# Kernel optimization log

Hardware: AMD Instinct MI355X
Metric: run time of the kernel (lower is better)

Reference implementation:

```python
import jax, jax.numpy as jnp
import numpy as np

B, S, D, N = 8, 4096, 1024, 64
EPS = 1e-5


def setup_inputs() -> dict:
    key = jax.random.key(0)
    ks = jax.random.split(key, 6)
    sD = 1.0 / np.sqrt(D)
    sN = 1.0 / np.sqrt(N)
    return {
        "x": jax.random.normal(ks[0], (B, S, D), dtype=jnp.float32),
        "ln_w": jnp.ones((D,), jnp.float32),
        "ln_b": jnp.zeros((D,), jnp.float32),
        "Wi": jax.random.normal(ks[1], (N, D), jnp.float32) * sD,
        "bi": jnp.zeros((N,), jnp.float32),
        "Wf": jax.random.normal(ks[2], (N, D), jnp.float32) * sD,
        "bf": jnp.zeros((N,), jnp.float32),
        "Wz": jax.random.normal(ks[3], (N, D), jnp.float32) * sD,
        "bz": jnp.zeros((N,), jnp.float32),
        "Wo": jax.random.normal(ks[4], (N, D), jnp.float32) * sD,
        "bo": jnp.zeros((N,), jnp.float32),
        "Wp": jax.random.normal(ks[5], (D, N), jnp.float32) * sN,
        "bp": jnp.zeros((D,), jnp.float32),
    }


def reference(x, ln_w, ln_b, Wi, bi, Wf, bf, Wz, bz, Wo, bo, Wp, bp):
    # LayerNorm over last dim (eps matches torch default 1e-5)
    mu = jnp.mean(x, axis=-1, keepdims=True)
    var = jnp.mean(jnp.square(x - mu), axis=-1, keepdims=True)
    xn = (x - mu) * jax.lax.rsqrt(var + EPS) * ln_w + ln_b

    # Precompute all four projections as batched GEMMs: (B,S,N)
    log_i = jnp.clip(jnp.einsum('bsd,nd->bsn', xn, Wi) + bi, -20.0, 20.0)
    log_f = jnp.clip(jnp.einsum('bsd,nd->bsn', xn, Wf) + bf, -20.0, 20.0)
    z = jnp.tanh(jnp.einsum('bsd,nd->bsn', xn, Wz) + bz)
    o = jax.nn.sigmoid(jnp.einsum('bsd,nd->bsn', xn, Wo) + bo)

    # Stabilized exponential-gated recurrence via lax.scan over time
    def step(carry, inp):
        c, m = carry
        li, lf, zt, ot = inp
        m_new = jnp.maximum(m + lf, li)
        i_s = jnp.exp(li - m_new)
        f_s = jnp.exp(m + lf - m_new)
        c = f_s * c + i_s * zt
        h = ot * jnp.tanh(c)
        return (c, m_new), h

    c0 = jnp.zeros((x.shape[0], log_i.shape[-1]), x.dtype)
    m0 = jnp.zeros_like(c0)
    # time-major inputs: (S,B,N)
    tm = lambda a: jnp.swapaxes(a, 0, 1)
    _, h_seq = jax.lax.scan(step, (c0, m0), (tm(log_i), tm(log_f), tm(z), tm(o)))
    h_seq = jnp.swapaxes(h_seq, 0, 1)  # (B,S,N)

    return jnp.einsum('bsn,dn->bsd', h_seq, Wp) + bp
```

## Files before the change

kernel.cpp:

```cpp
#include <hip/hip_runtime.h>
#include <hip/hip_bf16.h>

#define BB 8
#define SS 4096
#define DD 1024
#define NN 64
#define ROWS (BB * SS)
#define GLD 256
#define NCHUNK 256
#define CLEN 16

typedef _Float16 f16;
using f16x8 = __attribute__((ext_vector_type(8))) _Float16;
using f32x4 = __attribute__((ext_vector_type(4))) float;

__global__ __launch_bounds__(256) void prep_all(const float* __restrict__ Wi, const float* __restrict__ bi,
                                                const float* __restrict__ Wf, const float* __restrict__ bfv,
                                                const float* __restrict__ Wz, const float* __restrict__ bz,
                                                const float* __restrict__ Wo, const float* __restrict__ bo,
                                                const float* __restrict__ Wp,
                                                const float* __restrict__ ln_w, const float* __restrict__ ln_b,
                                                f16* __restrict__ Wpk, f16* __restrict__ Wpf,
                                                float* __restrict__ ball, float* __restrict__ e_all) {
    if (blockIdx.x < 384) {
        int i = blockIdx.x * 256 + threadIdx.x;
        if (i < 32768) {
            int l = i & 63, cb = (i >> 6) & 15, s = i >> 10;
            int r = cb * 16 + (l & 15);
            int c = s * 32 + (l >> 4) * 8;
            int g = r >> 6, rem = r & 63;
            const float* W = (g == 0) ? Wi : (g == 1) ? Wf : (g == 2) ? Wz : Wo;
            const float* src = W + rem * 1024 + c;
            const float* lwp = ln_w + c;
            f16x8 v;
            #pragma unroll
            for (int e = 0; e < 8; ++e) v[e] = (f16)(src[e] * lwp[e]);
            *reinterpret_cast<f16x8*>(Wpk + (size_t)s * 8192 + cb * 512 + l * 8) = v;
        } else if (i < 32768 + 65536) {
            int j = i - 32768;
            Wpf[j] = (f16)Wp[j];
        }
    } else {
        int j = (blockIdx.x - 384) * 4 + (threadIdx.x >> 6);
        int lane = threadIdx.x & 63;
        int g = j >> 6, rem = j & 63;
        const float* W  = (g == 0) ? Wi : (g == 1) ? Wf : (g == 2) ? Wz : Wo;
        const float* bs = (g == 0) ? bi : (g == 1) ? bfv : (g == 2) ? bz : bo;
        const float* row = W + rem * 1024;
        float d = 0.0f, e = 0.0f;
        #pragma unroll
        for (int t = 0; t < 16; ++t) {
            int k = lane + 64 * t;
            float w = row[k];
            e += ln_w[k] * w;
            d += ln_b[k] * w;
        }
        #pragma unroll
        for (int off = 1; off < 64; off <<= 1) {
            e += __shfl_xor(e, off);
            d += __shfl_xor(d, off);
        }
        if (lane == 0) { ball[j] = bs[rem] + d; e_all[j] = e; }
    }
}

__global__ __launch_bounds__(512, 1) void gate_gemm(const float* __restrict__ x,
                                                    const f16* __restrict__ Wpk,
                                                    const float* __restrict__ ball,
                                                    const float* __restrict__ e_all,
                                                    float* __restrict__ gates,
                                                    float4* __restrict__ s4) {
    int bm = blockIdx.x * 128;
    int tid = threadIdx.x;
    int wid = tid >> 6, lane = tid & 63;
    int wm = wid >> 2, wn = wid & 3;
    int lrow = lane & 15, lkg = lane >> 4;
    int srow = tid >> 2, skg = tid & 3;

    __shared__ __align__(16) char ldsbuf[98304];
    __shared__ float2 stats_lds[128];

    const float4* xrow = reinterpret_cast<const float4*>(x + (size_t)(bm + srow) * DD) + skg * 4;
    float4 A0, A1, A2, A3, B0, B1, B2, B3;
    uint4 W0, W1, W2, W3;
    const uint4* wsrc = reinterpret_cast<const uint4*>(Wpk) + wid * 256 + lane;

    auto loadA = [&](int s) { const float4* p = xrow + s * 16; A0 = p[0]; A1 = p[1]; A2 = p[2]; A3 = p[3]; };
    auto loadB = [&](int s) { const float4* p = xrow + s * 16; B0 = p[0]; B1 = p[1]; B2 = p[2]; B3 = p[3]; };
    auto loadW = [&](int s) { const uint4* p = wsrc + (size_t)s * 2048; W0 = p[0]; W1 = p[64]; W2 = p[128]; W3 = p[192]; };
    auto writeW = [&](int buf) {
        uint4* d = reinterpret_cast<uint4*>(ldsbuf + buf * 32768 + wid * 4096) + lane;
        d[0] = W0; d[64] = W1; d[128] = W2; d[192] = W3;
    };

    float s1 = 0.0f, s2 = 0.0f;
    auto writeXv = [&](float4 v0, float4 v1, float4 v2, float4 v3, int buf) {
        float xv[16] = {v0.x, v0.y, v0.z, v0.w, v1.x, v1.y, v1.z, v1.w,
                        v2.x, v2.y, v2.z, v2.w, v3.x, v3.y, v3.z, v3.w};
        f16x8 p0, p1;
        #pragma unroll
        for (int e = 0; e < 8; ++e) {
            s1 += xv[e] + xv[8 + e];
            s2 += xv[e] * xv[e] + xv[8 + e] * xv[8 + e];
            p0[e] = (f16)xv[e];
            p1[e] = (f16)xv[8 + e];
        }
        char* base = ldsbuf + 65536 + buf * 16384 + srow * 128;
        int r7 = srow & 7;
        *reinterpret_cast<f16x8*>(base + 16 * ((2 * skg) ^ r7))     = p0;
        *reinterpret_cast<f16x8*>(base + 16 * ((2 * skg + 1) ^ r7)) = p1;
    };

    f32x4 acc[4][4] = {};
    auto compute = [&](int buf) {
        #pragma unroll
        for (int h = 0; h < 2; ++h) {
            f16x8 a[4];
            #pragma unroll
            for (int mf = 0; mf < 4; ++mf) {
                int row = wm * 64 + mf * 16 + lrow;
                a[mf] = *reinterpret_cast<const f16x8*>(
                    ldsbuf + 65536 + buf * 16384 + row * 128 + 16 * ((4 * h + lkg) ^ (row & 7)));
            }
            #pragma unroll
            for (int nf = 0; nf < 4; ++nf) {
                int cb = wn * 4 + nf;
                f16x8 w = *reinterpret_cast<const f16x8*>(
                    ldsbuf + buf * 32768 + h * 16384 + cb * 1024 + lane * 16);
                #pragma unroll
                for (int mf = 0; mf < 4; ++mf)
                    acc[mf][nf] = __builtin_amdgcn_mfma_f32_16x16x32_f16(a[mf], w, acc[mf][nf], 0, 0, 0);
            }
        }
    };
    auto stepSync = [&]() {
        asm volatile("s_waitcnt lgkmcnt(0)" ::: "memory");
        __builtin_amdgcn_s_barrier();
        __builtin_amdgcn_sched_barrier(0);
    };

    loadA(0); loadB(1); loadW(0);
    writeW(0);
    writeXv(A0, A1, A2, A3, 0);
    loadA(2); loadW(1);
    stepSync();

    for (int it = 0; it < 8; ++it) {
        int s = 2 * it;
        compute(0);
        writeW(1);
        writeXv(B0, B1, B2, B3, 1);
        if (s + 2 <= 15) loadW(s + 2);
        if (s + 3 <= 15) loadB(s + 3);
        stepSync();
        compute(1);
        if (s + 2 <= 15) {
            writeW(0);
            writeXv(A0, A1, A2, A3, 0);
        }
        if (s + 3 <= 15) loadW(s + 3);
        if (s + 4 <= 15) loadA(s + 4);
        stepSync();
    }

    s1 += __shfl_xor(s1, 1); s2 += __shfl_xor(s2, 1);
    s1 += __shfl_xor(s1, 2); s2 += __shfl_xor(s2, 2);
    if ((tid & 3) == 0) {
        float mu = s1 * (1.0f / DD);
        float var = s2 * (1.0f / DD) - mu * mu;
        float rsd = rsqrtf(var + 1e-5f);
        float2 st; st.x = mu * rsd; st.y = rsd;
        stats_lds[srow] = st;
    }
    __syncthreads();

    float* glds = reinterpret_cast<float*>(ldsbuf);
    int c0 = wn * 64;
    int rb = (lane >> 4) * 4;
    #pragma unroll
    for (int mf = 0; mf < 4; ++mf) {
        #pragma unroll
        for (int nf = 0; nf < 4; ++nf) {
            int col = c0 + nf * 16 + (lane & 15);
            float bc = ball[col];
            float ec = e_all[col];
            #pragma unroll
            for (int r = 0; r < 4; ++r) {
                int rl = wm * 64 + mf * 16 + rb + r;
                float2 st = stats_lds[rl];
                float v = acc[mf][nf][r] * st.y + bc - st.x * ec;
                float res;
                if (wn == 0 || wn == 1)      res = fminf(fmaxf(v, -20.0f), 20.0f);
                else if (wn == 2)            res = tanhf(v);
                else                         res = 1.0f / (1.0f + expf(-v));
                gates[(size_t)(bm + rl) * GLD + col] = res;
                if (wn < 3)
                    glds[rl * 192 + col] = res;
            }
        }
    }
    __syncthreads();

    int b = bm >> 12;
    int cb0 = (bm & 4095) >> 4;
    {
        int lr0 = wid * 16;
        float Lf = 0.0f, m = -1e30f, c = 0.0f;
        #pragma unroll
        for (int j = 0; j < 16; ++j) {
            const float* g = glds + (lr0 + j) * 192;
            float li = g[lane], lf = g[64 + lane], z = g[128 + lane];
            Lf += lf;
            float ma = m + lf;
            float mn = fmaxf(ma, li);
            c = __expf(ma - mn) * c + __expf(li - mn) * z;
            m = mn;
        }
        float4 v; v.x = Lf; v.y = m; v.z = c; v.w = 0.0f;
        s4[(size_t)(b * NCHUNK + cb0 + wid) * 64 + lane] = v;
    }
}

__global__ __launch_bounds__(64) void scan_b(const float4* __restrict__ s4,
                                             float2* __restrict__ c2) {
    int b = blockIdx.x;
    int n = threadIdx.x;
    size_t base = (size_t)b * NCHUNK * 64 + n;
    float c = 0.0f, m = 0.0f;
    float4 cur[16];
    #pragma unroll
    for (int d = 0; d < 16; ++d) cur[d] = s4[base + (size_t)d * 64];
    for (int kb = 0; kb < NCHUNK; kb += 16) {
        float4 nxt[16];
        if (kb + 16 < NCHUNK) {
            #pragma unroll
            for (int d = 0; d < 16; ++d) nxt[d] = s4[base + (size_t)(kb + 16 + d) * 64];
        }
        #pragma unroll
        for (int d = 0; d < 16; ++d) {
            float2 ci; ci.x = m; ci.y = c;
            c2[base + (size_t)(kb + d) * 64] = ci;
            float4 v = cur[d];
            float ma = m + v.x;
            float mo = fmaxf(ma, v.y);
            c = expf(ma - mo) * c + expf(v.y - mo) * v.z;
            m = mo;
        }
        #pragma unroll
        for (int d = 0; d < 16; ++d) cur[d] = nxt[d];
    }
}

__global__ __launch_bounds__(256) void scan_c(const float* __restrict__ gates,
                                              const float2* __restrict__ c2,
                                              f16* __restrict__ h) {
    int w = blockIdx.x * 4 + (threadIdx.x >> 6);
    int lane = threadIdx.x & 63;
    int b = w >> 8, k = w & (NCHUNK - 1);
    int t0 = k * CLEN;
    float2 ci = c2[(size_t)(b * NCHUNK + k) * 64 + lane];
    float m = ci.x, c = ci.y;
    const float* gp = gates + ((size_t)(b * SS + t0)) * GLD + lane;
    f16* hp = h + ((size_t)(b * SS + t0)) * NN + lane;
    for (int t = 0; t < CLEN; ++t) {
        float li = gp[0], lf = gp[64], z = gp[128], o = gp[192];
        gp += GLD;
        float ma = m + lf;
        float mn = fmaxf(ma, li);
        c = expf(ma - mn) * c + expf(li - mn) * z;
        m = mn;
        *hp = (f16)(o * tanhf(c));
        hp += NN;
    }
}

__global__ __launch_bounds__(256) void out_gemm(const f16* __restrict__ h,
                                                const f16* __restrict__ Wpf,
                                                const float* __restrict__ bp,
                                                float* __restrict__ out) {
    int tid = threadIdx.x, wid = tid >> 6, lane = tid & 63;
    int r0 = (blockIdx.x >> 1) * 32;
    int c0 = (blockIdx.x & 1) * 512 + wid * 128;
    int lrow = lane & 15, lk = (lane >> 4) * 8;

    f32x4 acc[2][8] = {};
    #pragma unroll
    for (int ks = 0; ks < 2; ++ks) {
        int kk = ks * 32;
        f16x8 a[2], bfr[8];
        #pragma unroll
        for (int mf = 0; mf < 2; ++mf)
            a[mf] = *reinterpret_cast<const f16x8*>(h + (size_t)(r0 + mf * 16 + lrow) * NN + kk + lk);
        #pragma unroll
        for (int nf = 0; nf < 8; ++nf)
            bfr[nf] = *reinterpret_cast<const f16x8*>(Wpf + (size_t)(c0 + nf * 16 + lrow) * NN + kk + lk);
        #pragma unroll
        for (int mf = 0; mf < 2; ++mf)
            #pragma unroll
            for (int nf = 0; nf < 8; ++nf)
                acc[mf][nf] = __builtin_amdgcn_mfma_f32_16x16x32_f16(a[mf], bfr[nf], acc[mf][nf], 0, 0, 0);
    }
    int rb = (lane >> 4) * 4;
    #pragma unroll
    for (int nf = 0; nf < 8; ++nf) {
        int col = c0 + nf * 16 + (lane & 15);
        float bias = bp[col];
        #pragma unroll
        for (int mf = 0; mf < 2; ++mf) {
            #pragma unroll
            for (int r = 0; r < 4; ++r) {
                int row = r0 + mf * 16 + rb + r;
                out[(size_t)row * DD + col] = acc[mf][nf][r] + bias;
            }
        }
    }
}

extern "C" void kernel_launch(void* const* d_in, const int* in_sizes, int n_in,
                              void* d_out, int out_size, void* d_ws, size_t ws_size,
                              hipStream_t stream) {
    const float* x    = (const float*)d_in[0];
    const float* ln_w = (const float*)d_in[1];
    const float* ln_b = (const float*)d_in[2];
    const float* Wi   = (const float*)d_in[3];
    const float* bi   = (const float*)d_in[4];
    const float* Wf   = (const float*)d_in[5];
    const float* bfv  = (const float*)d_in[6];
    const float* Wz   = (const float*)d_in[7];
    const float* bz   = (const float*)d_in[8];
    const float* Wo   = (const float*)d_in[9];
    const float* bo   = (const float*)d_in[10];
    const float* Wp   = (const float*)d_in[11];
    const float* bp   = (const float*)d_in[12];
    float* out = (float*)d_out;

    char* w = (char*)d_ws;
    float* gates = (float*)w;  w += (size_t)ROWS * GLD * 4;
    float4* s4   = (float4*)w; w += (size_t)BB * NCHUNK * 64 * 16;
    float2* c2   = (float2*)w; w += (size_t)BB * NCHUNK * 64 * 8;
    f16* h       = (f16*)w;    w += (size_t)ROWS * NN * 2;
    f16* Wpk     = (f16*)w;    w += 32 * 8192 * 2;
    f16* Wpf     = (f16*)w;    w += 1024 * 64 * 2;
    float* ball  = (float*)w;  w += 256 * 4;
    float* e_all = (float*)w;  w += 256 * 4;

    prep_all<<<448, 256, 0, stream>>>(Wi, bi, Wf, bfv, Wz, bz, Wo, bo, Wp,
                                      ln_w, ln_b, Wpk, Wpf, ball, e_all);
    gate_gemm<<<ROWS / 128, 512, 0, stream>>>(x, Wpk, ball, e_all, gates, s4);
    scan_b<<<BB, 64, 0, stream>>>(s4, c2);
    scan_c<<<(BB * NCHUNK) / 4, 256, 0, stream>>>(gates, c2, h);
    out_gemm<<<(ROWS / 32) * 2, 256, 0, stream>>>(h, Wpf, bp, out);
}
```

Baseline: 139.7 us.

## Shrink gate GEMM tile to 64 rows, load weights directly to registers

The gate GEMM block goes from 128 rows with 512 threads to 64 rows with 256 threads and launch bounds allowing 3 blocks per CU. The K step drops to 32 and the loop runs 32 steps. Weight fragments are now loaded from global memory straight into registers instead of being staged through LDS. The X tile uses a smaller XOR swizzle, and the gate scratch row stride is padded to 194 floats to cut bank conflicts. The goal is higher occupancy and less LDS traffic, at the cost of more global weight loads per block and more barriers.

```diff
diff --git a/kernel.cpp b/kernel.cpp
--- a/kernel.cpp
+++ b/kernel.cpp
@@ -9,6 +9,7 @@
 #define GLD 256
 #define NCHUNK 256
 #define CLEN 16
+#define GST 194
 
 typedef _Float16 f16;
 using f16x8 = __attribute__((ext_vector_type(8))) _Float16;
@@ -64,74 +65,67 @@
     }
 }
 
-__global__ __launch_bounds__(512, 1) void gate_gemm(const float* __restrict__ x,
+__global__ __launch_bounds__(256, 3) void gate_gemm(const float* __restrict__ x,
                                                     const f16* __restrict__ Wpk,
                                                     const float* __restrict__ ball,
                                                     const float* __restrict__ e_all,
                                                     float* __restrict__ gates,
                                                     float4* __restrict__ s4) {
-    int bm = blockIdx.x * 128;
+    int bm = blockIdx.x * 64;
     int tid = threadIdx.x;
-    int wid = tid >> 6, lane = tid & 63;
-    int wm = wid >> 2, wn = wid & 3;
+    int wn = tid >> 6, lane = tid & 63;
     int lrow = lane & 15, lkg = lane >> 4;
     int srow = tid >> 2, skg = tid & 3;
 
-    __shared__ __align__(16) char ldsbuf[98304];
-    __shared__ float2 stats_lds[128];
-
-    const float4* xrow = reinterpret_cast<const float4*>(x + (size_t)(bm + srow) * DD) + skg * 4;
-    float4 A0, A1, A2, A3, B0, B1, B2, B3;
-    uint4 W0, W1, W2, W3;
-    const uint4* wsrc = reinterpret_cast<const uint4*>(Wpk) + wid * 256 + lane;
-
-    auto loadA = [&](int s) { const float4* p = xrow + s * 16; A0 = p[0]; A1 = p[1]; A2 = p[2]; A3 = p[3]; };
-    auto loadB = [&](int s) { const float4* p = xrow + s * 16; B0 = p[0]; B1 = p[1]; B2 = p[2]; B3 = p[3]; };
-    auto loadW = [&](int s) { const uint4* p = wsrc + (size_t)s * 2048; W0 = p[0]; W1 = p[64]; W2 = p[128]; W3 = p[192]; };
-    auto writeW = [&](int buf) {
-        uint4* d = reinterpret_cast<uint4*>(ldsbuf + buf * 32768 + wid * 4096) + lane;
-        d[0] = W0; d[64] = W1; d[128] = W2; d[192] = W3;
+    __shared__ __align__(16) char ldsbuf[64 * GST * 4];
+    __shared__ float2 stats_lds[64];
+
+    const float4* xrow = reinterpret_cast<const float4*>(x + (size_t)(bm + srow) * DD) + skg * 2;
+    const f16* wsrc = Wpk + wn * 4 * 512 + lane * 8;
+
+    float4 XA0, XA1, XB0, XB1;
+    f16x8 WA[4], WB[4];
+
+    auto loadXA = [&](int s) { XA0 = xrow[s * 8]; XA1 = xrow[s * 8 + 1]; };
+    auto loadXB = [&](int s) { XB0 = xrow[s * 8]; XB1 = xrow[s * 8 + 1]; };
+    auto loadWA = [&](int s) {
+        const f16* p = wsrc + (size_t)s * 8192;
+        #pragma unroll
+        for (int nf = 0; nf < 4; ++nf) WA[nf] = *reinterpret_cast<const f16x8*>(p + nf * 512);
+    };
+    auto loadWB = [&](int s) {
+        const f16* p = wsrc + (size_t)s * 8192;
+        #pragma unroll
+        for (int nf = 0; nf < 4; ++nf) WB[nf] = *reinterpret_cast<const f16x8*>(p + nf * 512);
     };
 
     float s1 = 0.0f, s2 = 0.0f;
-    auto writeXv = [&](float4 v0, float4 v1, float4 v2, float4 v3, int buf) {
-        float xv[16] = {v0.x, v0.y, v0.z, v0.w, v1.x, v1.y, v1.z, v1.w,
-                        v2.x, v2.y, v2.z, v2.w, v3.x, v3.y, v3.z, v3.w};
-        f16x8 p0, p1;
+    int wslot = (skg ^ ((srow >> 1) & 3)) << 4;
+    auto writeX = [&](float4 v0, float4 v1, int buf) {
+        float xv[8] = {v0.x, v0.y, v0.z, v0.w, v1.x, v1.y, v1.z, v1.w};
+        f16x8 p;
         #pragma unroll
         for (int e = 0; e < 8; ++e) {
-            s1 += xv[e] + xv[8 + e];
-            s2 += xv[e] * xv[e] + xv[8 + e] * xv[8 + e];
-            p0[e] = (f16)xv[e];
-            p1[e] = (f16)xv[8 + e];
-        }
-        char* base = ldsbuf + 65536 + buf * 16384 + srow * 128;
-        int r7 = srow & 7;
-        *reinterpret_cast<f16x8*>(base + 16 * ((2 * skg) ^ r7))     = p0;
-        *reinterpret_cast<f16x8*>(base + 16 * ((2 * skg + 1) ^ r7)) = p1;
+            s1 += xv[e]; s2 += xv[e] * xv[e];
+            p[e] = (f16)xv[e];
+        }
+        *reinterpret_cast<f16x8*>(ldsbuf + buf * 4096 + srow * 64 + wslot) = p;
     };
 
     f32x4 acc[4][4] = {};
-    auto compute = [&](int buf) {
-        #pragma unroll
-        for (int h = 0; h < 2; ++h) {
-            f16x8 a[4];
-            #pragma unroll
-            for (int mf = 0; mf < 4; ++mf) {
-                int row = wm * 64 + mf * 16 + lrow;
-                a[mf] = *reinterpret_cast<const f16x8*>(
-                    ldsbuf + 65536 + buf * 16384 + row * 128 + 16 * ((4 * h + lkg) ^ (row & 7)));
-            }
-            #pragma unroll
-            for (int nf = 0; nf < 4; ++nf) {
-                int cb = wn * 4 + nf;
-                f16x8 w = *reinterpret_cast<const f16x8*>(
-                    ldsbuf + buf * 32768 + h * 16384 + cb * 1024 + lane * 16);
-                #pragma unroll
-                for (int mf = 0; mf < 4; ++mf)
-                    acc[mf][nf] = __builtin_amdgcn_mfma_f32_16x16x32_f16(a[mf], w, acc[mf][nf], 0, 0, 0);
-            }
-        }
+    auto compute = [&](int buf, f16x8 (&W)[4]) {
+        f16x8 a[4];
+        #pragma unroll
+        for (int mf = 0; mf < 4; ++mf) {
+            int row = mf * 16 + lrow;
+            int slot = (lkg ^ ((row >> 1) & 3)) << 4;
+            a[mf] = *reinterpret_cast<const f16x8*>(ldsbuf + buf * 4096 + row * 64 + slot);
+        }
+        #pragma unroll
+        for (int nf = 0; nf < 4; ++nf)
+            #pragma unroll
+            for (int mf = 0; mf < 4; ++mf)
+                acc[mf][nf] = __builtin_amdgcn_mfma_f32_16x16x32_f16(a[mf], W[nf], acc[mf][nf], 0, 0, 0);
     };
     auto stepSync = [&]() {
         asm volatile("s_waitcnt lgkmcnt(0)" ::: "memory");
@@ -139,27 +133,23 @@
         __builtin_amdgcn_sched_barrier(0);
     };
 
-    loadA(0); loadB(1); loadW(0);
-    writeW(0);
-    writeXv(A0, A1, A2, A3, 0);
-    loadA(2); loadW(1);
+    loadXA(0); loadWA(0);
+    loadXB(1); loadWB(1);
+    writeX(XA0, XA1, 0);
+    loadXA(2);
     stepSync();
 
-    for (int it = 0; it < 8; ++it) {
+    for (int it = 0; it < 16; ++it) {
         int s = 2 * it;
-        compute(0);
-        writeW(1);
-        writeXv(B0, B1, B2, B3, 1);
-        if (s + 2 <= 15) loadW(s + 2);
-        if (s + 3 <= 15) loadB(s + 3);
+        compute(0, WA);
+        if (s + 2 < 32) loadWA(s + 2);
+        writeX(XB0, XB1, 1);
+        if (s + 3 < 32) loadXB(s + 3);
         stepSync();
-        compute(1);
-        if (s + 2 <= 15) {
-            writeW(0);
-            writeXv(A0, A1, A2, A3, 0);
-        }
-        if (s + 3 <= 15) loadW(s + 3);
-        if (s + 4 <= 15) loadA(s + 4);
+        compute(1, WB);
+        if (s + 3 < 32) loadWB(s + 3);
+        if (s + 2 < 32) writeX(XA0, XA1, 0);
+        if (s + 4 < 32) loadXA(s + 4);
         stepSync();
     }
 
@@ -186,7 +176,7 @@
             float ec = e_all[col];
             #pragma unroll
             for (int r = 0; r < 4; ++r) {
-                int rl = wm * 64 + mf * 16 + rb + r;
+                int rl = mf * 16 + rb + r;
                 float2 st = stats_lds[rl];
                 float v = acc[mf][nf][r] * st.y + bc - st.x * ec;
                 float res;
@@ -195,7 +185,7 @@
                 else                         res = 1.0f / (1.0f + expf(-v));
                 gates[(size_t)(bm + rl) * GLD + col] = res;
                 if (wn < 3)
-                    glds[rl * 192 + col] = res;
+                    glds[rl * GST + col] = res;
             }
         }
     }
@@ -204,11 +194,11 @@
     int b = bm >> 12;
     int cb0 = (bm & 4095) >> 4;
     {
-        int lr0 = wid * 16;
+        int lr0 = wn * 16;
         float Lf = 0.0f, m = -1e30f, c = 0.0f;
         #pragma unroll
         for (int j = 0; j < 16; ++j) {
-            const float* g = glds + (lr0 + j) * 192;
+            const float* g = glds + (lr0 + j) * GST;
             float li = g[lane], lf = g[64 + lane], z = g[128 + lane];
             Lf += lf;
             float ma = m + lf;
@@ -217,7 +207,7 @@
             m = mn;
         }
         float4 v; v.x = Lf; v.y = m; v.z = c; v.w = 0.0f;
-        s4[(size_t)(b * NCHUNK + cb0 + wid) * 64 + lane] = v;
+        s4[(size_t)(b * NCHUNK + cb0 + wn) * 64 + lane] = v;
     }
 }
 
@@ -346,7 +336,7 @@
 
     prep_all<<<448, 256, 0, stream>>>(Wi, bi, Wf, bfv, Wz, bz, Wo, bo, Wp,
                                       ln_w, ln_b, Wpk, Wpf, ball, e_all);
-    gate_gemm<<<ROWS / 128, 512, 0, stream>>>(x, Wpk, ball, e_all, gates, s4);
+    gate_gemm<<<ROWS / 64, 256, 0, stream>>>(x, Wpk, ball, e_all, gates, s4);
     scan_b<<<BB, 64, 0, stream>>>(s4, c2);
     scan_c<<<(BB * NCHUNK) / 4, 256, 0, stream>>>(gates, c2, h);
     out_gemm<<<(ROWS / 32) * 2, 256, 0, stream>>>(h, Wpf, bp, out);
```

Measured after the change: 144.2 us. +3.2%, slower.

## Use async global-to-LDS loads in gate GEMM, split N across blocks, separate chunk scan

Applied to the files above, without the earlier changes.

The gate GEMM now stages fp32 x tiles and packed fp16 weights straight into LDS with global_load_lds async copies. The f16 conversion and LayerNorm statistics move into the compute step. Each 128-row tile is split into two blocks over the 256 gate columns, using 256 threads with two blocks per CU, and the weight packing layout is changed to match. The per-chunk scan summary that was fused into the GEMM epilogue moves to a separate scan_a kernel that re-reads gates from global memory. This trades an extra launch and extra gate traffic for better load/compute overlap and occupancy, and x is now read twice (once per N-half).

```diff
diff --git a/kernel.cpp b/kernel.cpp
--- a/kernel.cpp
+++ b/kernel.cpp
@@ -13,6 +13,12 @@
 typedef _Float16 f16;
 using f16x8 = __attribute__((ext_vector_type(8))) _Float16;
 using f32x4 = __attribute__((ext_vector_type(4))) float;
+
+__device__ __forceinline__ void async16(void* lds, const void* g) {
+    __builtin_amdgcn_global_load_lds(
+        (const __attribute__((address_space(1))) unsigned int*)g,
+        (__attribute__((address_space(3))) unsigned int*)lds, 16, 0, 0);
+}
 
 __global__ __launch_bounds__(256) void prep_all(const float* __restrict__ Wi, const float* __restrict__ bi,
                                                 const float* __restrict__ Wf, const float* __restrict__ bfv,
@@ -25,17 +31,17 @@
     if (blockIdx.x < 384) {
         int i = blockIdx.x * 256 + threadIdx.x;
         if (i < 32768) {
-            int l = i & 63, cb = (i >> 6) & 15, s = i >> 10;
-            int r = cb * 16 + (l & 15);
-            int c = s * 32 + (l >> 4) * 8;
-            int g = r >> 6, rem = r & 63;
+            int l = i & 63, cb = (i >> 6) & 7, bn = (i >> 9) & 1, s = i >> 10;
+            int col = bn * 128 + cb * 16 + (l & 15);
+            int k = s * 32 + (l >> 4) * 8;
+            int g = col >> 6, rem = col & 63;
             const float* W = (g == 0) ? Wi : (g == 1) ? Wf : (g == 2) ? Wz : Wo;
-            const float* src = W + rem * 1024 + c;
-            const float* lwp = ln_w + c;
+            const float* src = W + rem * 1024 + k;
+            const float* lwp = ln_w + k;
             f16x8 v;
             #pragma unroll
             for (int e = 0; e < 8; ++e) v[e] = (f16)(src[e] * lwp[e]);
-            *reinterpret_cast<f16x8*>(Wpk + (size_t)s * 8192 + cb * 512 + l * 8) = v;
+            *reinterpret_cast<f16x8*>(Wpk + (size_t)s * 8192 + bn * 4096 + cb * 512 + l * 8) = v;
         } else if (i < 32768 + 65536) {
             int j = i - 32768;
             Wpf[j] = (f16)Wp[j];
@@ -64,124 +70,103 @@
     }
 }
 
-__global__ __launch_bounds__(512, 1) void gate_gemm(const float* __restrict__ x,
+__global__ __launch_bounds__(256, 2) void gate_gemm(const float* __restrict__ x,
                                                     const f16* __restrict__ Wpk,
                                                     const float* __restrict__ ball,
                                                     const float* __restrict__ e_all,
-                                                    float* __restrict__ gates,
-                                                    float4* __restrict__ s4) {
-    int bm = blockIdx.x * 128;
+                                                    float* __restrict__ gates) {
+    int bmi = blockIdx.x >> 1, bn = blockIdx.x & 1;
+    int bm = bmi * 128;
     int tid = threadIdx.x;
     int wid = tid >> 6, lane = tid & 63;
-    int wm = wid >> 2, wn = wid & 3;
+    int wm = wid >> 1, wn = wid & 1;
     int lrow = lane & 15, lkg = lane >> 4;
-    int srow = tid >> 2, skg = tid & 3;
-
-    __shared__ __align__(16) char ldsbuf[98304];
+
+    __shared__ __align__(16) char lds[2][24576];
     __shared__ float2 stats_lds[128];
 
-    const float4* xrow = reinterpret_cast<const float4*>(x + (size_t)(bm + srow) * DD) + skg * 4;
-    float4 A0, A1, A2, A3, B0, B1, B2, B3;
-    uint4 W0, W1, W2, W3;
-    const uint4* wsrc = reinterpret_cast<const uint4*>(Wpk) + wid * 256 + lane;
-
-    auto loadA = [&](int s) { const float4* p = xrow + s * 16; A0 = p[0]; A1 = p[1]; A2 = p[2]; A3 = p[3]; };
-    auto loadB = [&](int s) { const float4* p = xrow + s * 16; B0 = p[0]; B1 = p[1]; B2 = p[2]; B3 = p[3]; };
-    auto loadW = [&](int s) { const uint4* p = wsrc + (size_t)s * 2048; W0 = p[0]; W1 = p[64]; W2 = p[128]; W3 = p[192]; };
-    auto writeW = [&](int buf) {
-        uint4* d = reinterpret_cast<uint4*>(ldsbuf + buf * 32768 + wid * 4096) + lane;
-        d[0] = W0; d[64] = W1; d[128] = W2; d[192] = W3;
+    auto stage = [&](int s, int buf) {
+        #pragma unroll
+        for (int i = 0; i < 6; ++i) {
+            int d = wid * 6144 + i * 1024 + lane * 16;
+            char* dst = &lds[buf][d];
+            const char* src;
+            if (d < 16384) {
+                int row = d >> 7;
+                int col16 = ((d >> 4) & 7) ^ (row & 7);
+                src = (const char*)x + (size_t)(bm + row) * 4096 + s * 128 + col16 * 16;
+            } else {
+                src = (const char*)Wpk + (size_t)s * 16384 + bn * 8192 + (d - 16384);
+            }
+            async16(dst, src);
+        }
     };
 
-    float s1 = 0.0f, s2 = 0.0f;
-    auto writeXv = [&](float4 v0, float4 v1, float4 v2, float4 v3, int buf) {
-        float xv[16] = {v0.x, v0.y, v0.z, v0.w, v1.x, v1.y, v1.z, v1.w,
-                        v2.x, v2.y, v2.z, v2.w, v3.x, v3.y, v3.z, v3.w};
-        f16x8 p0, p1;
-        #pragma unroll
-        for (int e = 0; e < 8; ++e) {
-            s1 += xv[e] + xv[8 + e];
-            s2 += xv[e] * xv[e] + xv[8 + e] * xv[8 + e];
-            p0[e] = (f16)xv[e];
-            p1[e] = (f16)xv[8 + e];
-        }
-        char* base = ldsbuf + 65536 + buf * 16384 + srow * 128;
-        int r7 = srow & 7;
-        *reinterpret_cast<f16x8*>(base + 16 * ((2 * skg) ^ r7))     = p0;
-        *reinterpret_cast<f16x8*>(base + 16 * ((2 * skg + 1) ^ r7)) = p1;
+    f32x4 acc[4][4] = {};
+    float s1[4] = {}, s2[4] = {};
+    auto compute = [&](int buf) {
+        f16x8 a[4];
+        #pragma unroll
+        for (int mf = 0; mf < 4; ++mf) {
+            int row = wm * 64 + mf * 16 + lrow;
+            const char* rb_ = &lds[buf][row * 128];
+            int r7 = row & 7;
+            float4 q0 = *reinterpret_cast<const float4*>(rb_ + (((2 * lkg) ^ r7) << 4));
+            float4 q1 = *reinterpret_cast<const float4*>(rb_ + (((2 * lkg + 1) ^ r7) << 4));
+            if (wn == 0) {
+                s1[mf] += q0.x + q0.y + q0.z + q0.w + q1.x + q1.y + q1.z + q1.w;
+                s2[mf] += q0.x * q0.x + q0.y * q0.y + q0.z * q0.z + q0.w * q0.w
+                        + q1.x * q1.x + q1.y * q1.y + q1.z * q1.z + q1.w * q1.w;
+            }
+            f16x8 t;
+            t[0] = (f16)q0.x; t[1] = (f16)q0.y; t[2] = (f16)q0.z; t[3] = (f16)q0.w;
+            t[4] = (f16)q1.x; t[5] = (f16)q1.y; t[6] = (f16)q1.z; t[7] = (f16)q1.w;
+            a[mf] = t;
+        }
+        #pragma unroll
+        for (int nf = 0; nf < 4; ++nf) {
+            int cb = wn * 4 + nf;
+            f16x8 w = *reinterpret_cast<const f16x8*>(&lds[buf][16384 + cb * 1024 + lane * 16]);
+            #pragma unroll
+            for (int mf = 0; mf < 4; ++mf)
+                acc[mf][nf] = __builtin_amdgcn_mfma_f32_16x16x32_f16(a[mf], w, acc[mf][nf], 0, 0, 0);
+        }
     };
 
-    f32x4 acc[4][4] = {};
-    auto compute = [&](int buf) {
-        #pragma unroll
-        for (int h = 0; h < 2; ++h) {
-            f16x8 a[4];
-            #pragma unroll
-            for (int mf = 0; mf < 4; ++mf) {
+    stage(0, 0);
+    __syncthreads();
+    for (int s = 0; s < 32; ++s) {
+        int buf = s & 1;
+        if (s < 31) stage(s + 1, buf ^ 1);
+        compute(buf);
+        __syncthreads();
+    }
+
+    if (wn == 0) {
+        #pragma unroll
+        for (int mf = 0; mf < 4; ++mf) {
+            float a1 = s1[mf], a2 = s2[mf];
+            a1 += __shfl_xor(a1, 16); a2 += __shfl_xor(a2, 16);
+            a1 += __shfl_xor(a1, 32); a2 += __shfl_xor(a2, 32);
+            if (lane < 16) {
                 int row = wm * 64 + mf * 16 + lrow;
-                a[mf] = *reinterpret_cast<const f16x8*>(
-                    ldsbuf + 65536 + buf * 16384 + row * 128 + 16 * ((4 * h + lkg) ^ (row & 7)));
-            }
-            #pragma unroll
-            for (int nf = 0; nf < 4; ++nf) {
-                int cb = wn * 4 + nf;
-                f16x8 w = *reinterpret_cast<const f16x8*>(
-                    ldsbuf + buf * 32768 + h * 16384 + cb * 1024 + lane * 16);
-                #pragma unroll
-                for (int mf = 0; mf < 4; ++mf)
-                    acc[mf][nf] = __builtin_amdgcn_mfma_f32_16x16x32_f16(a[mf], w, acc[mf][nf], 0, 0, 0);
-            }
-        }
-    };
-    auto stepSync = [&]() {
-        asm volatile("s_waitcnt lgkmcnt(0)" ::: "memory");
-        __builtin_amdgcn_s_barrier();
-        __builtin_amdgcn_sched_barrier(0);
-    };
-
-    loadA(0); loadB(1); loadW(0);
-    writeW(0);
-    writeXv(A0, A1, A2, A3, 0);
-    loadA(2); loadW(1);
-    stepSync();
-
-    for (int it = 0; it < 8; ++it) {
-        int s = 2 * it;
-        compute(0);
-        writeW(1);
-        writeXv(B0, B1, B2, B3, 1);
-        if (s + 2 <= 15) loadW(s + 2);
-        if (s + 3 <= 15) loadB(s + 3);
-        stepSync();
-        compute(1);
-        if (s + 2 <= 15) {
-            writeW(0);
-            writeXv(A0, A1, A2, A3, 0);
-        }
-        if (s + 3 <= 15) loadW(s + 3);
-        if (s + 4 <= 15) loadA(s + 4);
-        stepSync();
-    }
-
-    s1 += __shfl_xor(s1, 1); s2 += __shfl_xor(s2, 1);
-    s1 += __shfl_xor(s1, 2); s2 += __shfl_xor(s2, 2);
-    if ((tid & 3) == 0) {
-        float mu = s1 * (1.0f / DD);
-        float var = s2 * (1.0f / DD) - mu * mu;
-        float rsd = rsqrtf(var + 1e-5f);
-        float2 st; st.x = mu * rsd; st.y = rsd;
-        stats_lds[srow] = st;
+                float mu = a1 * (1.0f / DD);
+                float var = a2 * (1.0f / DD) - mu * mu;
+                float rsd = rsqrtf(var + 1e-5f);
+                float2 st; st.x = mu * rsd; st.y = rsd;
+                stats_lds[row] = st;
+            }
+        }
     }
     __syncthreads();
 
-    float* glds = reinterpret_cast<float*>(ldsbuf);
-    int c0 = wn * 64;
+    int gidx = bn * 2 + wn;
     int rb = (lane >> 4) * 4;
     #pragma unroll
     for (int mf = 0; mf < 4; ++mf) {
         #pragma unroll
         for (int nf = 0; nf < 4; ++nf) {
-            int col = c0 + nf * 16 + (lane & 15);
+            int col = bn * 128 + wn * 64 + nf * 16 + lrow;
             float bc = ball[col];
             float ec = e_all[col];
             #pragma unroll
@@ -190,35 +175,34 @@
                 float2 st = stats_lds[rl];
                 float v = acc[mf][nf][r] * st.y + bc - st.x * ec;
                 float res;
-                if (wn == 0 || wn == 1)      res = fminf(fmaxf(v, -20.0f), 20.0f);
-                else if (wn == 2)            res = tanhf(v);
-                else                         res = 1.0f / (1.0f + expf(-v));
+                if (gidx < 2)           res = fminf(fmaxf(v, -20.0f), 20.0f);
+                else if (gidx == 2)     res = tanhf(v);
+                else                    res = 1.0f / (1.0f + expf(-v));
                 gates[(size_t)(bm + rl) * GLD + col] = res;
-                if (wn < 3)
-                    glds[rl * 192 + col] = res;
-            }
-        }
-    }
-    __syncthreads();
-
-    int b = bm >> 12;
-    int cb0 = (bm & 4095) >> 4;
-    {
-        int lr0 = wid * 16;
-        float Lf = 0.0f, m = -1e30f, c = 0.0f;
-        #pragma unroll
-        for (int j = 0; j < 16; ++j) {
-            const float* g = glds + (lr0 + j) * 192;
-            float li = g[lane], lf = g[64 + lane], z = g[128 + lane];
-            Lf += lf;
-            float ma = m + lf;
-            float mn = fmaxf(ma, li);
-            c = __expf(ma - mn) * c + __expf(li - mn) * z;
-            m = mn;
-        }
-        float4 v; v.x = Lf; v.y = m; v.z = c; v.w = 0.0f;
-        s4[(size_t)(b * NCHUNK + cb0 + wid) * 64 + lane] = v;
-    }
+            }
+        }
+    }
+}
+
+__global__ __launch_bounds__(256) void scan_a(const float* __restrict__ gates,
+                                              float4* __restrict__ s4) {
+    int w = blockIdx.x * 4 + (threadIdx.x >> 6);
+    int lane = threadIdx.x & 63;
+    int b = w >> 8, k = w & (NCHUNK - 1);
+    int t0 = k * CLEN;
+    const float* gp = gates + ((size_t)(b * SS + t0)) * GLD + lane;
+    float Lf = 0.0f, m = -1e30f, c = 0.0f;
+    for (int t = 0; t < CLEN; ++t) {
+        float li = gp[0], lf = gp[64], z = gp[128];
+        gp += GLD;
+        Lf += lf;
+        float ma = m + lf;
+        float mn = fmaxf(ma, li);
+        c = expf(ma - mn) * c + expf(li - mn) * z;
+        m = mn;
+    }
+    float4 v; v.x = Lf; v.y = m; v.z = c; v.w = 0.0f;
+    s4[(size_t)(b * NCHUNK + k) * 64 + lane] = v;
 }
 
 __global__ __launch_bounds__(64) void scan_b(const float4* __restrict__ s4,
@@ -346,7 +330,8 @@
 
     prep_all<<<448, 256, 0, stream>>>(Wi, bi, Wf, bfv, Wz, bz, Wo, bo, Wp,
                                       ln_w, ln_b, Wpk, Wpf, ball, e_all);
-    gate_gemm<<<ROWS / 128, 512, 0, stream>>>(x, Wpk, ball, e_all, gates, s4);
+    gate_gemm<<<512, 256, 0, stream>>>(x, Wpk, ball, e_all, gates);
+    scan_a<<<(BB * NCHUNK) / 4, 256, 0, stream>>>(gates, s4);
     scan_b<<<BB, 64, 0, stream>>>(s4, c2);
     scan_c<<<(BB * NCHUNK) / 4, 256, 0, stream>>>(gates, c2, h);
     out_gemm<<<(ROWS / 32) * 2, 256, 0, stream>>>(h, Wpf, bp, out);
```

Measured after the change: 158.9 us. 1.14x slower.
